# Performance work log

Hardware: AMD Instinct MI355X
Metric: run time of the kernel (lower is better)

## Reference

```python
import jax, jax.numpy as jnp
import numpy as np

E = 800000
D = 64
N = 50000

def setup_inputs() -> dict:
    key = jax.random.key(0)
    k1, k2 = jax.random.split(key)
    src = jax.random.normal(k1, (E, D), dtype=jnp.float32)
    index = jax.random.randint(k2, (E,), 0, N, dtype=jnp.int64)
    return {"src": src, "index": index, "dim": 0, "dim_size": N}

def reference(src, index, dim, dim_size):
    # scatter-mean along dim=0: segment sum divided by per-segment counts
    # (torch_scatter mean clamps count to >= 1 so empty segments stay 0).
    sums = jax.ops.segment_sum(src, index, num_segments=dim_size)  # [N, D]
    counts = jax.ops.segment_sum(jnp.ones((src.shape[0],), dtype=src.dtype),
                                 index, num_segments=dim_size)      # [N]
    denom = jnp.maximum(counts, 1.0)
    return sums / denom[:, None]
```

## Files before the change

### kernel.cpp

```cpp
#include <hip/hip_runtime.h>


typedef unsigned int u32;

__global__ void zero_u32_kernel(u32* __restrict__ p, int n) {
    int i = blockIdx.x * blockDim.x + threadIdx.x;
    int stride = gridDim.x * blockDim.x;
    for (; i < n; i += stride) p[i] = 0u;
}

__global__ void hist_rank_kernel(const int* __restrict__ idx, u32* __restrict__ hist,
                                 u32* __restrict__ rank, int E) {
    int i = blockIdx.x * blockDim.x + threadIdx.x;
    int stride = gridDim.x * blockDim.x;
    for (; i < E; i += stride) {
        rank[i] = atomicAdd(&hist[idx[i]], 1u);
    }
}


__global__ void scanA_kernel(const u32* __restrict__ hist, u32* __restrict__ pb, int N) {
    const int b = blockIdx.x, t = threadIdx.x;
    const int base = b * 1024 + t * 4;
    u32 s = 0;
#pragma unroll
    for (int k = 0; k < 4; ++k) { int i = base + k; if (i < N) s += hist[i]; }
#pragma unroll
    for (int d = 32; d > 0; d >>= 1) s += __shfl_down(s, d);
    __shared__ u32 wsum[4];
    int lane = t & 63, wid = t >> 6;
    if (lane == 0) wsum[wid] = s;
    __syncthreads();
    if (t == 0) pb[b] = wsum[0] + wsum[1] + wsum[2] + wsum[3];
}

__global__ void scanB_kernel(u32* __restrict__ pb, u32* __restrict__ ofs, int nblk, int N) {
    if (threadIdx.x == 0 && blockIdx.x == 0) {
        u32 run = 0;
        for (int b = 0; b < nblk; ++b) { u32 v = pb[b]; pb[b] = run; run += v; }
        ofs[N] = run;
    }
}

__global__ void scanC_kernel(const u32* __restrict__ hist, const u32* __restrict__ pb,
                             u32* __restrict__ ofs, int N) {
    const int b = blockIdx.x, t = threadIdx.x;
    const int base = b * 1024 + t * 4;
    u32 v[4]; u32 s = 0;
#pragma unroll
    for (int k = 0; k < 4; ++k) { int i = base + k; v[k] = (i < N) ? hist[i] : 0u; s += v[k]; }
    u32 inc = s;
    int lane = t & 63, wid = t >> 6;
#pragma unroll
    for (int d = 1; d < 64; d <<= 1) { u32 x = __shfl_up(inc, d); if (lane >= d) inc += x; }
    __shared__ u32 wsum[4];
    if (lane == 63) wsum[wid] = inc;
    __syncthreads();
    u32 waveBase = 0;
    for (int w = 0; w < wid; ++w) waveBase += wsum[w];
    u32 run = pb[b] + waveBase + (inc - s);
#pragma unroll
    for (int k = 0; k < 4; ++k) { int i = base + k; if (i < N) ofs[i] = run; run += v[k]; }
}

__global__ void scatter_perm_kernel(const int* __restrict__ idx, const u32* __restrict__ rank,
                                    const u32* __restrict__ ofs, u32* __restrict__ perm, int E) {
    int i = blockIdx.x * blockDim.x + threadIdx.x;
    int stride = gridDim.x * blockDim.x;
    for (; i < E; i += stride) {
        int n = idx[i];
        perm[ofs[n] + rank[i]] = (u32)i;
    }
}

__global__ void gather_mean_kernel(const float4* __restrict__ src4, const u32* __restrict__ perm,
                                   const u32* __restrict__ ofs, float4* __restrict__ out4, int N) {
    int seg = blockIdx.x * (blockDim.x >> 6) + (threadIdx.x >> 6);
    if (seg >= N) return;
    int lane = threadIdx.x & 63;
    int g = lane >> 4;
    int q = lane & 15;
    u32 beg = ofs[seg], end = ofs[seg + 1];
    int cnt = (int)(end - beg);
    float4 acc = make_float4(0.f, 0.f, 0.f, 0.f);
    int j = 0;
    while (j < cnt) {
        int chunk = cnt - j; if (chunk > 64) chunk = 64;
        u32 myperm = (lane < chunk) ? perm[beg + j + lane] : 0u;
        int k = 0;
        for (; k + 8 <= chunk; k += 8) {
            u32 eA = __shfl(myperm, k + g);
            u32 eB = __shfl(myperm, k + 4 + g);
            float4 vA = src4[(long)eA * 16 + q];
            float4 vB = src4[(long)eB * 16 + q];
            acc.x += vA.x + vB.x; acc.y += vA.y + vB.y;
            acc.z += vA.z + vB.z; acc.w += vA.w + vB.w;
        }
        for (; k < chunk; k += 4) {
            int r = k + g;
            u32 e = __shfl(myperm, r < chunk ? r : k);
            if (r < chunk) {
                float4 v = src4[(long)e * 16 + q];
                acc.x += v.x; acc.y += v.y; acc.z += v.z; acc.w += v.w;
            }
        }
        j += chunk;
    }
    acc.x += __shfl_down(acc.x, 32); acc.y += __shfl_down(acc.y, 32);
    acc.z += __shfl_down(acc.z, 32); acc.w += __shfl_down(acc.w, 32);
    acc.x += __shfl_down(acc.x, 16); acc.y += __shfl_down(acc.y, 16);
    acc.z += __shfl_down(acc.z, 16); acc.w += __shfl_down(acc.w, 16);
    if (g == 0) {
        float inv = 1.0f / (float)(cnt > 1 ? cnt : 1);
        acc.x *= inv; acc.y *= inv; acc.z *= inv; acc.w *= inv;
        out4[(long)seg * 16 + q] = acc;
    }
}

__global__ void zero_f4_kernel(float4* __restrict__ p, long n4) {
    long i = (long)blockIdx.x * blockDim.x + threadIdx.x;
    long stride = (long)gridDim.x * blockDim.x;
    float4 z = make_float4(0.f, 0.f, 0.f, 0.f);
    for (; i < n4; i += stride) p[i] = z;
}
__global__ void scatter_add_kernel(const float4* __restrict__ src4, const int* __restrict__ idx,
                                   float* __restrict__ out, float* __restrict__ cnt, int E) {
    long t = (long)blockIdx.x * blockDim.x + threadIdx.x;
    long total = (long)E * 16;
    long stride = (long)gridDim.x * blockDim.x;
    for (; t < total; t += stride) {
        int e = (int)(t >> 4), c4 = (int)(t & 15);
        int n = idx[e];
        float4 v = src4[(long)e * 16 + c4];
        float* o = out + (long)n * 64 + c4 * 4;
        atomicAdd(o + 0, v.x); atomicAdd(o + 1, v.y);
        atomicAdd(o + 2, v.z); atomicAdd(o + 3, v.w);
        if (c4 == 0) atomicAdd(cnt + n, 1.0f);
    }
}
__global__ void divide_kernel(float4* __restrict__ out4, const float* __restrict__ cnt, int N) {
    long t = (long)blockIdx.x * blockDim.x + threadIdx.x;
    long total = (long)N * 16;
    long stride = (long)gridDim.x * blockDim.x;
    for (; t < total; t += stride) {
        int n = (int)(t >> 4);
        float inv = 1.0f / fmaxf(cnt[n], 1.0f);
        float4 v = out4[t];
        v.x *= inv; v.y *= inv; v.z *= inv; v.w *= inv;
        out4[t] = v;
    }
}

extern "C" void kernel_launch(void* const* d_in, const int* in_sizes, int n_in,
                              void* d_out, int out_size, void* d_ws, size_t ws_size,
                              hipStream_t stream) {
    const float* src = (const float*)d_in[0];
    const int*   idx = (const int*)d_in[1];
    float* out = (float*)d_out;

    const int E = in_sizes[1];
    const int D = in_sizes[0] / E;
    const int N = out_size / D;
    const int BLK = 256;

    const size_t OFS_OFF  = 0;
    const size_t HIST_OFF = ((size_t)(N + 1) + 63) & ~63ul;
    const size_t PB_OFF   = HIST_OFF + (((size_t)N + 63) & ~63ul);
    const size_t RANK_OFF = PB_OFF + 64;
    const size_t PERM_OFF = RANK_OFF + (size_t)E;
    const size_t NEED = (PERM_OFF + (size_t)E) * 4;

    if (ws_size >= NEED) {
        u32* W    = (u32*)d_ws;
        u32* ofs  = W + OFS_OFF;
        u32* hist = W + HIST_OFF;
        u32* pb   = W + PB_OFF;
        u32* rank = W + RANK_OFF;
        u32* perm = W + PERM_OFF;

        const int nblk = (N + 1023) / 1024;

        {
            int grid = (N + BLK - 1) / BLK;
            zero_u32_kernel<<<grid, BLK, 0, stream>>>(hist, N);
        }
        {
            int grid = (E + BLK - 1) / BLK;
            hist_rank_kernel<<<grid, BLK, 0, stream>>>(idx, hist, rank, E);
        }
        scanA_kernel<<<nblk, BLK, 0, stream>>>(hist, pb, N);
        scanB_kernel<<<1, 64, 0, stream>>>(pb, ofs, nblk, N);
        scanC_kernel<<<nblk, BLK, 0, stream>>>(hist, pb, ofs, N);
        {
            int grid = (E + BLK - 1) / BLK;
            scatter_perm_kernel<<<grid, BLK, 0, stream>>>(idx, rank, ofs, perm, E);
        }
        {
            int segs_per_blk = BLK / 64;
            int grid = (N + segs_per_blk - 1) / segs_per_blk;
            gather_mean_kernel<<<grid, BLK, 0, stream>>>((const float4*)src, perm, ofs,
                                                         (float4*)out, N);
        }
    } else {
        float* cnt = (float*)d_ws;
        {
            long n4 = (long)out_size / 4;
            int grid = (int)((n4 + BLK - 1) / BLK); if (grid > 2048) grid = 2048;
            zero_f4_kernel<<<grid, BLK, 0, stream>>>((float4*)out, n4);
        }
        {
            long n4 = (long)N / 4;
            int grid = (int)((n4 + BLK - 1) / BLK); if (grid > 2048) grid = 2048;
            zero_f4_kernel<<<grid, BLK, 0, stream>>>((float4*)cnt, n4);
        }
        {
            long total = (long)E * 16;
            int grid = (int)((total + BLK - 1) / BLK); if (grid > 2048) grid = 2048;
            scatter_add_kernel<<<grid, BLK, 0, stream>>>((const float4*)src, idx, out, cnt, E);
        }
        {
            long total = (long)N * 16;
            int grid = (int)((total + BLK - 1) / BLK); if (grid > 2048) grid = 2048;
            divide_kernel<<<grid, BLK, 0, stream>>>((float4*)out, cnt, N);
        }
    }
}
```

Before: 353.0 us.

## Replace CSR histogram-scan-permute build with fixed-capacity per-segment slot buckets

Segment grouping moves from a histogram, three scan kernels and a permutation scatter to a single atomic pass. That pass writes each edge index into a fixed 128-entry bucket for its segment, and entries past capacity go to a bounded overflow list. The gather kernel reads bucket contents directly, and a small fix-up kernel atomically adds the overflow edges scaled by the inverse count. This drops several launches and the rank and offset traffic. In exchange it needs a much larger workspace (N×128 words), which may push execution onto the atomic fallback path. It also silently drops edges if more than 4096 overflow.

```diff
diff --git a/kernel.cpp b/kernel.cpp
--- a/kernel.cpp
+++ b/kernel.cpp
@@ -2,6 +2,9 @@
 
 
 typedef unsigned int u32;
+
+#define CAP 128
+#define OVF_MAX 4096
 
 __global__ void zero_u32_kernel(u32* __restrict__ p, int n) {
     int i = blockIdx.x * blockDim.x + threadIdx.x;
@@ -9,84 +12,37 @@
     for (; i < n; i += stride) p[i] = 0u;
 }
 
-__global__ void hist_rank_kernel(const int* __restrict__ idx, u32* __restrict__ hist,
-                                 u32* __restrict__ rank, int E) {
-    int i = blockIdx.x * blockDim.x + threadIdx.x;
-    int stride = gridDim.x * blockDim.x;
-    for (; i < E; i += stride) {
-        rank[i] = atomicAdd(&hist[idx[i]], 1u);
-    }
-}
-
-
-__global__ void scanA_kernel(const u32* __restrict__ hist, u32* __restrict__ pb, int N) {
-    const int b = blockIdx.x, t = threadIdx.x;
-    const int base = b * 1024 + t * 4;
-    u32 s = 0;
-#pragma unroll
-    for (int k = 0; k < 4; ++k) { int i = base + k; if (i < N) s += hist[i]; }
-#pragma unroll
-    for (int d = 32; d > 0; d >>= 1) s += __shfl_down(s, d);
-    __shared__ u32 wsum[4];
-    int lane = t & 63, wid = t >> 6;
-    if (lane == 0) wsum[wid] = s;
-    __syncthreads();
-    if (t == 0) pb[b] = wsum[0] + wsum[1] + wsum[2] + wsum[3];
-}
-
-__global__ void scanB_kernel(u32* __restrict__ pb, u32* __restrict__ ofs, int nblk, int N) {
-    if (threadIdx.x == 0 && blockIdx.x == 0) {
-        u32 run = 0;
-        for (int b = 0; b < nblk; ++b) { u32 v = pb[b]; pb[b] = run; run += v; }
-        ofs[N] = run;
-    }
-}
-
-__global__ void scanC_kernel(const u32* __restrict__ hist, const u32* __restrict__ pb,
-                             u32* __restrict__ ofs, int N) {
-    const int b = blockIdx.x, t = threadIdx.x;
-    const int base = b * 1024 + t * 4;
-    u32 v[4]; u32 s = 0;
-#pragma unroll
-    for (int k = 0; k < 4; ++k) { int i = base + k; v[k] = (i < N) ? hist[i] : 0u; s += v[k]; }
-    u32 inc = s;
-    int lane = t & 63, wid = t >> 6;
-#pragma unroll
-    for (int d = 1; d < 64; d <<= 1) { u32 x = __shfl_up(inc, d); if (lane >= d) inc += x; }
-    __shared__ u32 wsum[4];
-    if (lane == 63) wsum[wid] = inc;
-    __syncthreads();
-    u32 waveBase = 0;
-    for (int w = 0; w < wid; ++w) waveBase += wsum[w];
-    u32 run = pb[b] + waveBase + (inc - s);
-#pragma unroll
-    for (int k = 0; k < 4; ++k) { int i = base + k; if (i < N) ofs[i] = run; run += v[k]; }
-}
-
-__global__ void scatter_perm_kernel(const int* __restrict__ idx, const u32* __restrict__ rank,
-                                    const u32* __restrict__ ofs, u32* __restrict__ perm, int E) {
+__global__ void slot_scatter_kernel(const int* __restrict__ idx, u32* __restrict__ cnt,
+                                    u32* __restrict__ slot, u32* __restrict__ ovf, int E) {
     int i = blockIdx.x * blockDim.x + threadIdx.x;
     int stride = gridDim.x * blockDim.x;
     for (; i < E; i += stride) {
         int n = idx[i];
-        perm[ofs[n] + rank[i]] = (u32)i;
+        u32 pos = atomicAdd(&cnt[n], 1u);
+        if (pos < CAP) {
+            slot[(long)n * CAP + pos] = (u32)i;
+        } else {
+            u32 o = atomicAdd(&ovf[0], 1u);
+            if (o < OVF_MAX) ovf[1 + o] = (u32)i;
+        }
     }
 }
 
-__global__ void gather_mean_kernel(const float4* __restrict__ src4, const u32* __restrict__ perm,
-                                   const u32* __restrict__ ofs, float4* __restrict__ out4, int N) {
+__global__ void gather_mean_kernel(const float4* __restrict__ src4, const u32* __restrict__ slot,
+                                   const u32* __restrict__ cnt, float4* __restrict__ out4, int N) {
     int seg = blockIdx.x * (blockDim.x >> 6) + (threadIdx.x >> 6);
     if (seg >= N) return;
     int lane = threadIdx.x & 63;
     int g = lane >> 4;
     int q = lane & 15;
-    u32 beg = ofs[seg], end = ofs[seg + 1];
-    int cnt = (int)(end - beg);
+    int c = (int)cnt[seg];
+    int m = c < CAP ? c : CAP;
+    const u32* sl = slot + (long)seg * CAP;
     float4 acc = make_float4(0.f, 0.f, 0.f, 0.f);
     int j = 0;
-    while (j < cnt) {
-        int chunk = cnt - j; if (chunk > 64) chunk = 64;
-        u32 myperm = (lane < chunk) ? perm[beg + j + lane] : 0u;
+    while (j < m) {
+        int chunk = m - j; if (chunk > 64) chunk = 64;
+        u32 myperm = (lane < chunk) ? sl[j + lane] : 0u;
         int k = 0;
         for (; k + 8 <= chunk; k += 8) {
             u32 eA = __shfl(myperm, k + g);
@@ -111,9 +67,25 @@
     acc.x += __shfl_down(acc.x, 16); acc.y += __shfl_down(acc.y, 16);
     acc.z += __shfl_down(acc.z, 16); acc.w += __shfl_down(acc.w, 16);
     if (g == 0) {
-        float inv = 1.0f / (float)(cnt > 1 ? cnt : 1);
+        float inv = 1.0f / (float)(c > 1 ? c : 1);
         acc.x *= inv; acc.y *= inv; acc.z *= inv; acc.w *= inv;
         out4[(long)seg * 16 + q] = acc;
+    }
+}
+
+__global__ void ovf_fix_kernel(const float* __restrict__ src, const int* __restrict__ idx,
+                               const u32* __restrict__ cnt, const u32* __restrict__ ovf,
+                               float* __restrict__ out) {
+    u32 no = ovf[0]; if (no > OVF_MAX) no = OVF_MAX;
+    int nw = (gridDim.x * blockDim.x) >> 6;
+    int w  = (blockIdx.x * blockDim.x + threadIdx.x) >> 6;
+    int lane = threadIdx.x & 63;
+    for (u32 t = (u32)w; t < no; t += (u32)nw) {
+        u32 e = ovf[1 + t];
+        int n = idx[e];
+        u32 c = cnt[n];
+        float inv = 1.0f / (float)(c > 1u ? c : 1u);
+        atomicAdd(&out[(long)n * 64 + lane], src[(long)e * 64 + lane] * inv);
     }
 }
 
@@ -163,43 +135,34 @@
     const int N = out_size / D;
     const int BLK = 256;
 
-    const size_t OFS_OFF  = 0;
-    const size_t HIST_OFF = ((size_t)(N + 1) + 63) & ~63ul;
-    const size_t PB_OFF   = HIST_OFF + (((size_t)N + 63) & ~63ul);
-    const size_t RANK_OFF = PB_OFF + 64;
-    const size_t PERM_OFF = RANK_OFF + (size_t)E;
-    const size_t NEED = (PERM_OFF + (size_t)E) * 4;
+    const size_t CNT_OFF  = 0;
+    const size_t OVF_OFF  = ((size_t)N + 63) & ~63ul;
+    const size_t SLOT_OFF = (OVF_OFF + 1 + OVF_MAX + 127) & ~127ul;
+    const size_t NEED = (SLOT_OFF + (size_t)N * CAP) * 4;
 
     if (ws_size >= NEED) {
         u32* W    = (u32*)d_ws;
-        u32* ofs  = W + OFS_OFF;
-        u32* hist = W + HIST_OFF;
-        u32* pb   = W + PB_OFF;
-        u32* rank = W + RANK_OFF;
-        u32* perm = W + PERM_OFF;
-
-        const int nblk = (N + 1023) / 1024;
+        u32* cnt  = W + CNT_OFF;
+        u32* ovf  = W + OVF_OFF;
+        u32* slot = W + SLOT_OFF;
 
         {
-            int grid = (N + BLK - 1) / BLK;
-            zero_u32_kernel<<<grid, BLK, 0, stream>>>(hist, N);
+            int span = (int)(OVF_OFF - CNT_OFF) + 1;
+            int grid = (span + BLK - 1) / BLK;
+            zero_u32_kernel<<<grid, BLK, 0, stream>>>(cnt, span);
         }
         {
             int grid = (E + BLK - 1) / BLK;
-            hist_rank_kernel<<<grid, BLK, 0, stream>>>(idx, hist, rank, E);
-        }
-        scanA_kernel<<<nblk, BLK, 0, stream>>>(hist, pb, N);
-        scanB_kernel<<<1, 64, 0, stream>>>(pb, ofs, nblk, N);
-        scanC_kernel<<<nblk, BLK, 0, stream>>>(hist, pb, ofs, N);
-        {
-            int grid = (E + BLK - 1) / BLK;
-            scatter_perm_kernel<<<grid, BLK, 0, stream>>>(idx, rank, ofs, perm, E);
+            slot_scatter_kernel<<<grid, BLK, 0, stream>>>(idx, cnt, slot, ovf, E);
         }
         {
             int segs_per_blk = BLK / 64;
             int grid = (N + segs_per_blk - 1) / segs_per_blk;
-            gather_mean_kernel<<<grid, BLK, 0, stream>>>((const float4*)src, perm, ofs,
+            gather_mean_kernel<<<grid, BLK, 0, stream>>>((const float4*)src, slot, cnt,
                                                          (float4*)out, N);
+        }
+        {
+            ovf_fix_kernel<<<1, 256, 0, stream>>>(src, idx, cnt, ovf, out);
         }
     } else {
         float* cnt = (float*)d_ws;
```

New measurement: 352.1 us. Within noise of the previous version (-0.2%).
